# Kernel optimization log

Measured on AMD Instinct MI355X. Metric: run time of the kernel, lower is better.

The kernel has to match this reference:

```python
import jax, jax.numpy as jnp
import numpy as np

N_NODES = 1000000
N_EDGES = 32000000
NUM_GRAPHS = 1024


def setup_inputs() -> dict:
    key = jax.random.key(0)
    k1, k2, k3, k4, k5 = jax.random.split(key, 5)
    x = jax.random.normal(k1, (N_NODES, 1), dtype=jnp.float32)
    W = jax.random.normal(k2, (1, 1), dtype=jnp.float32)
    b = jax.random.normal(k3, (1,), dtype=jnp.float32)
    edge_index = jax.random.randint(k4, (2, N_EDGES), 0, N_NODES, dtype=jnp.int64)
    batch = jnp.sort(jax.random.randint(k5, (N_NODES,), 0, NUM_GRAPHS, dtype=jnp.int64))
    return {"x": x, "W": W, "b": b, "edge_index": edge_index, "batch": batch}


def reference(x, W, b, edge_index, batch):
    src, dst = edge_index[0], edge_index[1]
    # SimpleConv (default sum aggregation): out[i] = sum_{(j->i) in E} x[j]
    agg = jax.ops.segment_sum(x[src], dst, num_segments=N_NODES)  # [N,1]
    h = jax.nn.relu(agg)
    # global_mean_pool over graph ids
    sums = jax.ops.segment_sum(h, batch, num_segments=NUM_GRAPHS)  # [G,1]
    counts = jax.ops.segment_sum(jnp.ones((N_NODES,), dtype=h.dtype), batch,
                                 num_segments=NUM_GRAPHS)  # [G]
    pooled = sums / jnp.maximum(counts, 1.0)[:, None]
    # Linear(1 -> 1): y = pooled @ W^T + b
    return pooled @ W.T + b
```

## Files before the change

kernel.cpp:

```cpp
#include <hip/hip_runtime.h>

#define N_NODES    1000000
#define N_EDGES    32000000
#define NUM_GRAPHS 1024

typedef int          vint4  __attribute__((ext_vector_type(4)));
typedef unsigned int uint32;
typedef unsigned int vuint4 __attribute__((ext_vector_type(4)));

#define BUCKET_SHIFT 12
#define BUCKET_NODES (1 << BUCKET_SHIFT)
#define NBUCKETS     245

#define T1_NCHUNK   512
#define T1_BLOCK    512
#define T1_EDGES_PER_CHUNK (N_EDGES / T1_NCHUNK)
#define T1_PAIRS    (T1_EDGES_PER_CHUNK / 2)
#define T1_ROUNDS   ((T1_PAIRS + T1_BLOCK - 1) / T1_BLOCK)
#define SCAP        36
#define SLAB_CAP    368

#define T2_CAP      136192
#define T2_NCHUNK   512
#define T2_EPC      (N_EDGES / T2_NCHUNK)

__global__ __launch_bounds__(T1_BLOCK)
void slab_scatter(const int* __restrict__ src,
                  const int* __restrict__ dst,
                  uint32* __restrict__ slab,
                  uint32* __restrict__ fcnt_g,
                  uint32* __restrict__ ecnt_g) {
    __shared__ uint32 stage[NBUCKETS][SCAP];
    __shared__ uint32 rhist[NBUCKETS];
    __shared__ uint32 rpos[NBUCKETS];
    __shared__ uint32 ecnt[NBUCKETS];
    __shared__ uint32 flushed[NBUCKETS];
    __shared__ uint32 carry[NBUCKETS];

    const int tid = threadIdx.x;
    const int w   = blockIdx.x;
    const size_t ebase = (size_t)w * T1_EDGES_PER_CHUNK;
    const int2* d2 = (const int2*)(dst + ebase);
    const int2* s2 = (const int2*)(src + ebase);

    for (int b = tid; b < NBUCKETS; b += T1_BLOCK) {
        rhist[b] = 0; rpos[b] = 0; ecnt[b] = 0; flushed[b] = 0; carry[b] = 0;
    }
    __syncthreads();

    const int grp    = tid >> 4;
    const int lane16 = tid & 15;

    for (int r = 0; r < T1_ROUNDS; ++r) {
        int p = r * T1_BLOCK + tid;
        int b0 = -1, b1 = -1; uint32 v0 = 0, v1 = 0;
        if (p < T1_PAIRS) {
            int2 d = d2[p];
            int2 s = s2[p];
            b0 = (uint32)d.x >> BUCKET_SHIFT;
            v0 = (((uint32)d.x & (BUCKET_NODES - 1)) << 20) | (uint32)s.x;
            b1 = (uint32)d.y >> BUCKET_SHIFT;
            v1 = (((uint32)d.y & (BUCKET_NODES - 1)) << 20) | (uint32)s.y;
            atomicAdd(&rhist[b0], 1u);
            atomicAdd(&rhist[b1], 1u);
        }
        __syncthreads();
        if (p < T1_PAIRS) {
            if (carry[b0] + rhist[b0] <= SCAP) {
                uint32 c = atomicAdd(&rpos[b0], 1u);
                stage[b0][carry[b0] + c] = v0;
            } else {
                uint32 e = atomicAdd(&ecnt[b0], 1u);
                slab[((size_t)b0 * T1_NCHUNK + w) * SLAB_CAP + (SLAB_CAP - 1 - e)] = v0;
            }
            if (carry[b1] + rhist[b1] <= SCAP) {
                uint32 c = atomicAdd(&rpos[b1], 1u);
                stage[b1][carry[b1] + c] = v1;
            } else {
                uint32 e = atomicAdd(&ecnt[b1], 1u);
                slab[((size_t)b1 * T1_NCHUNK + w) * SLAB_CAP + (SLAB_CAP - 1 - e)] = v1;
            }
        }
        __syncthreads();
        for (int b = grp; b < NBUCKETS; b += 32) {
            uint32 car   = carry[b];
            uint32 tot   = car + rpos[b];
            uint32 lines = tot >> 4;
            uint32 rem   = tot & 15u;
            uint32 fl    = flushed[b];
            uint32* dp = slab + ((size_t)b * T1_NCHUNK + w) * SLAB_CAP + fl;
            for (uint32 l = 0; l < lines; ++l)
                dp[l * 16 + lane16] = stage[b][l * 16 + lane16];
            if (lines) {
                uint32 mv = 0;
                if (lane16 < rem) mv = stage[b][lines * 16 + lane16];
                if (lane16 < rem) stage[b][lane16] = mv;
            }
            if (lane16 == 0) {
                flushed[b] = fl + lines * 16;
                carry[b]   = rem;
                rpos[b]    = 0;
                rhist[b]   = 0;
            }
        }
        __syncthreads();
    }
    for (int b = grp; b < NBUCKETS; b += 32) {
        uint32 rem = carry[b];
        uint32 fl  = flushed[b];
        uint32* dp = slab + ((size_t)b * T1_NCHUNK + w) * SLAB_CAP + fl;
        if (lane16 < rem) dp[lane16] = stage[b][lane16];
        if (lane16 == 0) {
            fcnt_g[(size_t)b * T1_NCHUNK + w] = fl + rem;
            ecnt_g[(size_t)b * T1_NCHUNK + w] = ecnt[b];
        }
    }
}

__global__ __launch_bounds__(1024)
void slab_reduce(const uint32* __restrict__ slab,
                 const uint32* __restrict__ fcnt_g,
                 const uint32* __restrict__ ecnt_g,
                 const float* __restrict__ x,
                 const int* __restrict__ batch,
                 float* __restrict__ sums,
                 float* __restrict__ counts) {
    __shared__ float acc[BUCKET_NODES];
    const int b = blockIdx.x;
    const int tid = threadIdx.x;
    for (int n = tid; n < BUCKET_NODES; n += 1024) acc[n] = 0.0f;
    __syncthreads();

    const int wv = tid >> 6, lane = tid & 63;
    for (int w = wv; w < T1_NCHUNK; w += 16) {
        size_t cell = (size_t)b * T1_NCHUNK + w;
        uint32 fc = fcnt_g[cell];
        uint32 ec = ecnt_g[cell];
        const uint32* base = slab + cell * SLAB_CAP;
        for (uint32 i = lane; i < fc; i += 64) {
            uint32 v = base[i];
            atomicAdd(&acc[v >> 20], x[v & 0xFFFFFu]);
        }
        for (uint32 i = lane; i < ec; i += 64) {
            uint32 v = base[SLAB_CAP - 1 - i];
            atomicAdd(&acc[v >> 20], x[v & 0xFFFFFu]);
        }
    }
    __syncthreads();

    const int node0 = b << BUCKET_SHIFT;
    for (int n = tid; n < BUCKET_NODES; n += 1024) {
        int i = node0 + n;
        float h = 0.0f;
        int g = -1;
        if (i < N_NODES) {
            h = fmaxf(acc[n], 0.0f);
            g = batch[i];
        }
        int g0 = __shfl(g, 0);
        if (__all(g == g0)) {
            #pragma unroll
            for (int off = 32; off > 0; off >>= 1)
                h += __shfl_down(h, off);
            if ((tid & 63) == 0 && g0 >= 0) {
                atomicAdd(&sums[g0], h);
                atomicAdd(&counts[g0], 64.0f);
            }
        } else if (g >= 0) {
            atomicAdd(&sums[g], h);
            atomicAdd(&counts[g], 1.0f);
        }
    }
}

__global__ void finalize_kernel(const float* __restrict__ sums,
                                const float* __restrict__ counts,
                                const float* __restrict__ W,
                                const float* __restrict__ b,
                                float* __restrict__ out) {
    int g = blockIdx.x * blockDim.x + threadIdx.x;
    if (g < NUM_GRAPHS) {
        float pooled = sums[g] / fmaxf(counts[g], 1.0f);
        out[g] = pooled * W[0] + b[0];
    }
}

__global__ __launch_bounds__(1024)
void bucket_scatter(const int* __restrict__ src,
                    const int* __restrict__ dst,
                    uint32* __restrict__ sorted,
                    uint32* __restrict__ gpos) {
    __shared__ uint32 hist[NBUCKETS];
    __shared__ uint32 pos[NBUCKETS];
    const int tid = threadIdx.x;
    const size_t base = (size_t)blockIdx.x * T2_EPC;
    for (int b = tid; b < NBUCKETS; b += 1024) hist[b] = 0;
    __syncthreads();
    const vint4* d4 = (const vint4*)(dst + base);
    const vint4* s4 = (const vint4*)(src + base);
    const int nvec = T2_EPC / 4;
    for (int i = tid; i < nvec; i += 1024) {
        vint4 d = d4[i];
        atomicAdd(&hist[(uint32)d.x >> BUCKET_SHIFT], 1u);
        atomicAdd(&hist[(uint32)d.y >> BUCKET_SHIFT], 1u);
        atomicAdd(&hist[(uint32)d.z >> BUCKET_SHIFT], 1u);
        atomicAdd(&hist[(uint32)d.w >> BUCKET_SHIFT], 1u);
    }
    __syncthreads();
    for (int b = tid; b < NBUCKETS; b += 1024)
        pos[b] = atomicAdd(&gpos[b], hist[b]);
    __syncthreads();
    for (int i = tid; i < nvec; i += 1024) {
        vint4 d = d4[i];
        vint4 s = s4[i];
        {
            uint32 dd = (uint32)d.x, b = dd >> BUCKET_SHIFT, dl = dd & (BUCKET_NODES - 1);
            uint32 slot = atomicAdd(&pos[b], 1u);
            if (slot < T2_CAP) sorted[(size_t)b * T2_CAP + slot] = (dl << 20) | (uint32)s.x;
        }
        {
            uint32 dd = (uint32)d.y, b = dd >> BUCKET_SHIFT, dl = dd & (BUCKET_NODES - 1);
            uint32 slot = atomicAdd(&pos[b], 1u);
            if (slot < T2_CAP) sorted[(size_t)b * T2_CAP + slot] = (dl << 20) | (uint32)s.y;
        }
        {
            uint32 dd = (uint32)d.z, b = dd >> BUCKET_SHIFT, dl = dd & (BUCKET_NODES - 1);
            uint32 slot = atomicAdd(&pos[b], 1u);
            if (slot < T2_CAP) sorted[(size_t)b * T2_CAP + slot] = (dl << 20) | (uint32)s.z;
        }
        {
            uint32 dd = (uint32)d.w, b = dd >> BUCKET_SHIFT, dl = dd & (BUCKET_NODES - 1);
            uint32 slot = atomicAdd(&pos[b], 1u);
            if (slot < T2_CAP) sorted[(size_t)b * T2_CAP + slot] = (dl << 20) | (uint32)s.w;
        }
    }
}

__global__ __launch_bounds__(1024)
void bucket_reduce(const uint32* __restrict__ sorted,
                   const uint32* __restrict__ gpos,
                   const float* __restrict__ x,
                   const int* __restrict__ batch,
                   float* __restrict__ sums,
                   float* __restrict__ counts) {
    __shared__ float acc[BUCKET_NODES];
    const int b = blockIdx.x;
    const int tid = threadIdx.x;
    for (int n = tid; n < BUCKET_NODES; n += 1024) acc[n] = 0.0f;
    __syncthreads();
    uint32 cnt = gpos[b];
    if (cnt > T2_CAP) cnt = T2_CAP;
    const uint32* reg = sorted + (size_t)b * T2_CAP;
    const vuint4* r4 = (const vuint4*)reg;
    const uint32 nvec = cnt / 4;
    for (uint32 i = tid; i < nvec; i += 1024) {
        vuint4 v = r4[i];
        atomicAdd(&acc[v.x >> 20], x[v.x & 0xFFFFFu]);
        atomicAdd(&acc[v.y >> 20], x[v.y & 0xFFFFFu]);
        atomicAdd(&acc[v.z >> 20], x[v.z & 0xFFFFFu]);
        atomicAdd(&acc[v.w >> 20], x[v.w & 0xFFFFFu]);
    }
    for (uint32 i = nvec * 4 + tid; i < cnt; i += 1024) {
        uint32 v = reg[i];
        atomicAdd(&acc[v >> 20], x[v & 0xFFFFFu]);
    }
    __syncthreads();
    const int node0 = b << BUCKET_SHIFT;
    for (int n = tid; n < BUCKET_NODES; n += 1024) {
        int i = node0 + n;
        float h = 0.0f;
        int g = -1;
        if (i < N_NODES) {
            h = fmaxf(acc[n], 0.0f);
            g = batch[i];
        }
        int g0 = __shfl(g, 0);
        if (__all(g == g0)) {
            #pragma unroll
            for (int off = 32; off > 0; off >>= 1)
                h += __shfl_down(h, off);
            if ((tid & 63) == 0 && g0 >= 0) {
                atomicAdd(&sums[g0], h);
                atomicAdd(&counts[g0], 64.0f);
            }
        } else if (g >= 0) {
            atomicAdd(&sums[g], h);
            atomicAdd(&counts[g], 1.0f);
        }
    }
}

__global__ void scatter_edges_dev(const vint4* __restrict__ src4,
                                  const vint4* __restrict__ dst4,
                                  const float* __restrict__ x,
                                  float* __restrict__ agg) {
    int t = blockIdx.x * blockDim.x + threadIdx.x;
    if (t < N_EDGES / 4) {
        vint4 s = __builtin_nontemporal_load(&src4[t]);
        vint4 d = __builtin_nontemporal_load(&dst4[t]);
        atomicAdd(&agg[d.x], x[s.x]);
        atomicAdd(&agg[d.y], x[s.y]);
        atomicAdd(&agg[d.z], x[s.z]);
        atomicAdd(&agg[d.w], x[s.w]);
    }
}

__global__ void pool_nodes_kernel(const float* __restrict__ agg,
                                  const int* __restrict__ batch,
                                  float* __restrict__ sums,
                                  float* __restrict__ counts) {
    int i = blockIdx.x * blockDim.x + threadIdx.x;
    float h = 0.0f;
    int g = -1;
    if (i < N_NODES) {
        h = fmaxf(agg[i], 0.0f);
        g = batch[i];
    }
    int g0 = __shfl(g, 0);
    if (__all(g == g0)) {
        #pragma unroll
        for (int off = 32; off > 0; off >>= 1)
            h += __shfl_down(h, off);
        if ((threadIdx.x & 63) == 0 && g0 >= 0) {
            atomicAdd(&sums[g0], h);
            atomicAdd(&counts[g0], 64.0f);
        }
    } else if (g >= 0) {
        atomicAdd(&sums[g], h);
        atomicAdd(&counts[g], 1.0f);
    }
}

extern "C" void kernel_launch(void* const* d_in, const int* in_sizes, int n_in,
                              void* d_out, int out_size, void* d_ws, size_t ws_size,
                              hipStream_t stream) {
    const float* x     = (const float*)d_in[0];
    const float* W     = (const float*)d_in[1];
    const float* b     = (const float*)d_in[2];
    const int*   edge  = (const int*)d_in[3];
    const int*   batch = (const int*)d_in[4];
    float* out = (float*)d_out;

    const int* src = edge;
    const int* dst = edge + N_EDGES;

    const size_t ncells     = (size_t)NBUCKETS * T1_NCHUNK;
    const size_t slab_elems = ncells * SLAB_CAP;
    const size_t need1 = (slab_elems + 2 * ncells + 2 * NUM_GRAPHS) * 4;
    const size_t t2_elems = (size_t)NBUCKETS * T2_CAP;
    const size_t need2 = (t2_elems + 256 + 2 * NUM_GRAPHS) * 4;

    if (ws_size >= need1) {
        uint32* slab   = (uint32*)d_ws;
        uint32* fcnt_g = slab + slab_elems;
        uint32* ecnt_g = fcnt_g + ncells;
        float*  sums   = (float*)(ecnt_g + ncells);
        float*  counts = sums + NUM_GRAPHS;
        (void)hipMemsetAsync(sums, 0, 2 * NUM_GRAPHS * 4, stream);

        slab_scatter<<<T1_NCHUNK, T1_BLOCK, 0, stream>>>(src, dst, slab, fcnt_g, ecnt_g);
        slab_reduce<<<NBUCKETS, 1024, 0, stream>>>(slab, fcnt_g, ecnt_g, x, batch, sums, counts);
        finalize_kernel<<<(NUM_GRAPHS + 255) / 256, 256, 0, stream>>>(sums, counts, W, b, out);
    } else if (ws_size >= need2) {
        uint32* sorted = (uint32*)d_ws;
        uint32* gpos   = sorted + t2_elems;
        float*  sums   = (float*)(gpos + 256);
        float*  counts = sums + NUM_GRAPHS;
        (void)hipMemsetAsync(gpos, 0, (256 + 2 * NUM_GRAPHS) * 4, stream);

        bucket_scatter<<<T2_NCHUNK, 1024, 0, stream>>>(src, dst, sorted, gpos);
        bucket_reduce<<<NBUCKETS, 1024, 0, stream>>>(sorted, gpos, x, batch, sums, counts);
        finalize_kernel<<<(NUM_GRAPHS + 255) / 256, 256, 0, stream>>>(sums, counts, W, b, out);
    } else {
        float* agg    = (float*)d_ws;
        float* sums   = agg + N_NODES;
        float* counts = sums + NUM_GRAPHS;
        (void)hipMemsetAsync(d_ws, 0, ((size_t)N_NODES + 2 * NUM_GRAPHS) * 4, stream);

        int nthreads = N_EDGES / 4;
        scatter_edges_dev<<<(nthreads + 255) / 256, 256, 0, stream>>>(
            (const vint4*)src, (const vint4*)dst, x, agg);
        pool_nodes_kernel<<<(N_NODES + 255) / 256, 256, 0, stream>>>(agg, batch, sums, counts);
        finalize_kernel<<<(NUM_GRAPHS + 255) / 256, 256, 0, stream>>>(sums, counts, W, b, out);
    }
}
```

Measured before the change: 732.8 us.

## Process four edges per thread in slab scatter and drop per-round histogram pass

The slab scatter kernel now loads edges as int4 quads instead of pairs and enlarges the shared staging capacity per bucket. The separate histogram phase and its barrier are removed: each edge takes a slot via one atomic on the position counter, and edges past the staging capacity spill straight to the slab tail. The reduce kernel reads full slab entries as 4-wide vectors. The aim is fewer global load instructions, fewer barriers and fewer shared atomics per edge, at the cost of more shared memory per block and possibly more spill writes when a bucket overflows within a round.

```diff
diff --git a/kernel.cpp b/kernel.cpp
--- a/kernel.cpp
+++ b/kernel.cpp
@@ -15,9 +15,9 @@
 #define T1_NCHUNK   512
 #define T1_BLOCK    512
 #define T1_EDGES_PER_CHUNK (N_EDGES / T1_NCHUNK)
-#define T1_PAIRS    (T1_EDGES_PER_CHUNK / 2)
-#define T1_ROUNDS   ((T1_PAIRS + T1_BLOCK - 1) / T1_BLOCK)
-#define SCAP        36
+#define T1_QUADS    (T1_EDGES_PER_CHUNK / 4)
+#define T1_ROUNDS   ((T1_QUADS + T1_BLOCK - 1) / T1_BLOCK)
+#define SCAP        64
 #define SLAB_CAP    368
 
 #define T2_CAP      136192
@@ -31,7 +31,6 @@
                   uint32* __restrict__ fcnt_g,
                   uint32* __restrict__ ecnt_g) {
     __shared__ uint32 stage[NBUCKETS][SCAP];
-    __shared__ uint32 rhist[NBUCKETS];
     __shared__ uint32 rpos[NBUCKETS];
     __shared__ uint32 ecnt[NBUCKETS];
     __shared__ uint32 flushed[NBUCKETS];
@@ -39,12 +38,11 @@
 
     const int tid = threadIdx.x;
     const int w   = blockIdx.x;
-    const size_t ebase = (size_t)w * T1_EDGES_PER_CHUNK;
-    const int2* d2 = (const int2*)(dst + ebase);
-    const int2* s2 = (const int2*)(src + ebase);
+    const vint4* d4 = (const vint4*)(dst + (size_t)w * T1_EDGES_PER_CHUNK);
+    const vint4* s4 = (const vint4*)(src + (size_t)w * T1_EDGES_PER_CHUNK);
 
     for (int b = tid; b < NBUCKETS; b += T1_BLOCK) {
-        rhist[b] = 0; rpos[b] = 0; ecnt[b] = 0; flushed[b] = 0; carry[b] = 0;
+        rpos[b] = 0; ecnt[b] = 0; flushed[b] = 0; carry[b] = 0;
     }
     __syncthreads();
 
@@ -52,39 +50,29 @@
     const int lane16 = tid & 15;
 
     for (int r = 0; r < T1_ROUNDS; ++r) {
-        int p = r * T1_BLOCK + tid;
-        int b0 = -1, b1 = -1; uint32 v0 = 0, v1 = 0;
-        if (p < T1_PAIRS) {
-            int2 d = d2[p];
-            int2 s = s2[p];
-            b0 = (uint32)d.x >> BUCKET_SHIFT;
-            v0 = (((uint32)d.x & (BUCKET_NODES - 1)) << 20) | (uint32)s.x;
-            b1 = (uint32)d.y >> BUCKET_SHIFT;
-            v1 = (((uint32)d.y & (BUCKET_NODES - 1)) << 20) | (uint32)s.y;
-            atomicAdd(&rhist[b0], 1u);
-            atomicAdd(&rhist[b1], 1u);
-        }
-        __syncthreads();
-        if (p < T1_PAIRS) {
-            if (carry[b0] + rhist[b0] <= SCAP) {
-                uint32 c = atomicAdd(&rpos[b0], 1u);
-                stage[b0][carry[b0] + c] = v0;
-            } else {
-                uint32 e = atomicAdd(&ecnt[b0], 1u);
-                slab[((size_t)b0 * T1_NCHUNK + w) * SLAB_CAP + (SLAB_CAP - 1 - e)] = v0;
-            }
-            if (carry[b1] + rhist[b1] <= SCAP) {
-                uint32 c = atomicAdd(&rpos[b1], 1u);
-                stage[b1][carry[b1] + c] = v1;
-            } else {
-                uint32 e = atomicAdd(&ecnt[b1], 1u);
-                slab[((size_t)b1 * T1_NCHUNK + w) * SLAB_CAP + (SLAB_CAP - 1 - e)] = v1;
+        int q = r * T1_BLOCK + tid;
+        if (q < T1_QUADS) {
+            vint4 d = d4[q];
+            vint4 s = s4[q];
+            #pragma unroll
+            for (int k = 0; k < 4; ++k) {
+                uint32 dd = (uint32)(k == 0 ? d.x : k == 1 ? d.y : k == 2 ? d.z : d.w);
+                uint32 ss = (uint32)(k == 0 ? s.x : k == 1 ? s.y : k == 2 ? s.z : s.w);
+                uint32 b  = dd >> BUCKET_SHIFT;
+                uint32 v  = ((dd & (BUCKET_NODES - 1)) << 20) | ss;
+                uint32 c  = carry[b] + atomicAdd(&rpos[b], 1u);
+                if (c < SCAP) {
+                    stage[b][c] = v;
+                } else {
+                    uint32 e = atomicAdd(&ecnt[b], 1u);
+                    slab[((size_t)b * T1_NCHUNK + w) * SLAB_CAP + (SLAB_CAP - 1 - e)] = v;
+                }
             }
         }
         __syncthreads();
         for (int b = grp; b < NBUCKETS; b += 32) {
-            uint32 car   = carry[b];
-            uint32 tot   = car + rpos[b];
+            uint32 tot = carry[b] + rpos[b];
+            if (tot > SCAP) tot = SCAP;
             uint32 lines = tot >> 4;
             uint32 rem   = tot & 15u;
             uint32 fl    = flushed[b];
@@ -100,7 +88,6 @@
                 flushed[b] = fl + lines * 16;
                 carry[b]   = rem;
                 rpos[b]    = 0;
-                rhist[b]   = 0;
             }
         }
         __syncthreads();
@@ -137,7 +124,16 @@
         uint32 fc = fcnt_g[cell];
         uint32 ec = ecnt_g[cell];
         const uint32* base = slab + cell * SLAB_CAP;
-        for (uint32 i = lane; i < fc; i += 64) {
+        const vuint4* b4 = (const vuint4*)base;
+        uint32 nq = fc >> 2;
+        for (uint32 i = lane; i < nq; i += 64) {
+            vuint4 v = b4[i];
+            atomicAdd(&acc[v.x >> 20], x[v.x & 0xFFFFFu]);
+            atomicAdd(&acc[v.y >> 20], x[v.y & 0xFFFFFu]);
+            atomicAdd(&acc[v.z >> 20], x[v.z & 0xFFFFFu]);
+            atomicAdd(&acc[v.w >> 20], x[v.w & 0xFFFFFu]);
+        }
+        for (uint32 i = nq * 4 + lane; i < fc; i += 64) {
             uint32 v = base[i];
             atomicAdd(&acc[v >> 20], x[v & 0xFFFFFu]);
         }
@@ -213,25 +209,13 @@
     for (int i = tid; i < nvec; i += 1024) {
         vint4 d = d4[i];
         vint4 s = s4[i];
-        {
-            uint32 dd = (uint32)d.x, b = dd >> BUCKET_SHIFT, dl = dd & (BUCKET_NODES - 1);
+        #pragma unroll
+        for (int k = 0; k < 4; ++k) {
+            uint32 dd = (uint32)(k == 0 ? d.x : k == 1 ? d.y : k == 2 ? d.z : d.w);
+            uint32 ss = (uint32)(k == 0 ? s.x : k == 1 ? s.y : k == 2 ? s.z : s.w);
+            uint32 b = dd >> BUCKET_SHIFT, dl = dd & (BUCKET_NODES - 1);
             uint32 slot = atomicAdd(&pos[b], 1u);
-            if (slot < T2_CAP) sorted[(size_t)b * T2_CAP + slot] = (dl << 20) | (uint32)s.x;
-        }
-        {
-            uint32 dd = (uint32)d.y, b = dd >> BUCKET_SHIFT, dl = dd & (BUCKET_NODES - 1);
-            uint32 slot = atomicAdd(&pos[b], 1u);
-            if (slot < T2_CAP) sorted[(size_t)b * T2_CAP + slot] = (dl << 20) | (uint32)s.y;
-        }
-        {
-            uint32 dd = (uint32)d.z, b = dd >> BUCKET_SHIFT, dl = dd & (BUCKET_NODES - 1);
-            uint32 slot = atomicAdd(&pos[b], 1u);
-            if (slot < T2_CAP) sorted[(size_t)b * T2_CAP + slot] = (dl << 20) | (uint32)s.z;
-        }
-        {
-            uint32 dd = (uint32)d.w, b = dd >> BUCKET_SHIFT, dl = dd & (BUCKET_NODES - 1);
-            uint32 slot = atomicAdd(&pos[b], 1u);
-            if (slot < T2_CAP) sorted[(size_t)b * T2_CAP + slot] = (dl << 20) | (uint32)s.w;
+            if (slot < T2_CAP) sorted[(size_t)b * T2_CAP + slot] = (dl << 20) | ss;
         }
     }
 }
```

Measured after the change: 622.9 us. 1.18x faster.
